# Kernel tuning notes

Hardware: AMD Instinct MI355X
Metric: run time of the kernel (lower is better)

The kernel has to match this reference:

```python
import jax, jax.numpy as jnp
import numpy as np

B, T, E, H = 2, 2048, 1024, 16
D = E // H          # head_size = 64
DF = 4 * E          # FFN inner dim


def setup_inputs() -> dict:
    key = jax.random.key(0)
    ks = jax.random.split(key, 10)
    s = E ** -0.5
    return {
        "x":  jax.random.normal(ks[0], (B, T, E), jnp.float32),
        "Wq": jax.random.normal(ks[1], (H, E, D), jnp.float32) * s,
        "Wk": jax.random.normal(ks[2], (H, E, D), jnp.float32) * s,
        "Wv": jax.random.normal(ks[3], (H, E, D), jnp.float32) * s,
        "Wo": jax.random.normal(ks[4], (E, E), jnp.float32) * s,
        "bo": jnp.zeros((E,), jnp.float32),
        "W1": jax.random.normal(ks[5], (E, DF), jnp.float32) * s,
        "b1": jnp.zeros((DF,), jnp.float32),
        "W2": jax.random.normal(ks[6], (DF, E), jnp.float32) * (DF ** -0.5),
        "b2": jnp.zeros((E,), jnp.float32),
    }


def reference(x, Wq, Wk, Wv, Wo, bo, W1, b1, W2, b2):
    Bx, Tx, C = x.shape
    # NOTE: source scales by C**-0.5 where C = n_embed (not head_size) -- faithful.
    scale = C ** -0.5
    q = jnp.einsum('btc,hcd->bhtd', x, Wq)
    k = jnp.einsum('btc,hcd->bhtd', x, Wk)
    v = jnp.einsum('btc,hcd->bhtd', x, Wv)
    scores = jnp.einsum('bhtd,bhsd->bhts', q, k) * scale   # [B,H,T,T]
    causal = jnp.tril(jnp.ones((Tx, Tx), bool))
    scores = jnp.where(causal, scores, -jnp.inf)
    attn = jax.nn.softmax(scores, axis=-1)
    out = jnp.einsum('bhts,bhsd->bhtd', attn, v)
    out = out.transpose(0, 2, 1, 3).reshape(Bx, Tx, C)     # concat heads
    x = x + (out @ Wo + bo)                                # residual + projection
    h = jax.nn.relu(x @ W1 + b1)
    x = x + (h @ W2 + b2)                                  # residual + FFN
    return x
```

## Files before the change

kernel.cpp:

```cpp
#include <hip/hip_runtime.h>

#define B_ 2
#define T_ 2048
#define E_ 1024
#define H_ 16
#define D_ 64
#define DF_ 4096
#define M_ (B_*T_)
#define NQKV_ 3072

typedef unsigned short u16;
typedef __attribute__((ext_vector_type(8))) short short8;
typedef __attribute__((ext_vector_type(4))) float f32x4;
typedef __attribute__((ext_vector_type(16))) float f32x16;

__device__ __forceinline__ u16 f2bf(float f) {
  unsigned u = __builtin_bit_cast(unsigned, f);
  u += 0x7FFFu + ((u >> 16) & 1u);
  return (u16)(u >> 16);
}
__device__ __forceinline__ unsigned pack2bf(float a, float b) {
  return (unsigned)f2bf(a) | ((unsigned)f2bf(b) << 16);
}
__device__ __forceinline__ float bf2f(u16 u) {
  return __builtin_bit_cast(float, (unsigned)u << 16);
}

__device__ __forceinline__ void gload_lds16(const u16* g, u16* l) {
  __builtin_amdgcn_global_load_lds((const __attribute__((address_space(1))) void*)g,
                                   (__attribute__((address_space(3))) void*)l, 16, 0, 0);
}

__global__ __launch_bounds__(256) void cast_bf16_kernel(const float* __restrict__ in,
                                                        u16* __restrict__ out, int n4) {
  int i = blockIdx.x * 256 + threadIdx.x;
  if (i >= n4) return;
  float4 v = ((const float4*)in)[i];
  uint2 r;
  r.x = (unsigned)f2bf(v.x) | ((unsigned)f2bf(v.y) << 16);
  r.y = (unsigned)f2bf(v.z) | ((unsigned)f2bf(v.w) << 16);
  ((uint2*)out)[i] = r;
}

__global__ __launch_bounds__(256) void transpose_cast_kernel(const float* __restrict__ in,
                                                             u16* __restrict__ out,
                                                             int R, int C, int outld) {
  __shared__ float tile[32][33];
  int z = blockIdx.z;
  int c0 = blockIdx.x * 32, r0 = blockIdx.y * 32;
  int tx = threadIdx.x & 31, ty = threadIdx.x >> 5;
  const float* ip = in + (size_t)z * R * C;
#pragma unroll
  for (int i = 0; i < 32; i += 8)
    tile[ty + i][tx] = ip[(size_t)(r0 + ty + i) * C + (c0 + tx)];
  __syncthreads();
#pragma unroll
  for (int i = 0; i < 32; i += 8)
    out[(size_t)(z * C + c0 + ty + i) * outld + (r0 + tx)] = f2bf(tile[tx][ty + i]);
}

__global__ __launch_bounds__(256) void transpose_u16_kernel(const u16* __restrict__ in,
                                                            u16* __restrict__ out,
                                                            int R, int C, int ldin) {
  __shared__ __attribute__((aligned(16))) u16 tile[64][72];
  int c0 = blockIdx.x * 64, r0 = blockIdx.y * 64;
  int t = threadIdx.x;
  int tr = t >> 4, tc = (t & 15) * 4;
#pragma unroll
  for (int i = 0; i < 4; i++)
    *(uint2*)&tile[tr + i * 16][tc] = *(const uint2*)&in[(size_t)(r0 + tr + i * 16) * ldin + c0 + tc];
  __syncthreads();
  int rr = (t & 15) * 4, cc0 = t >> 4;
#pragma unroll
  for (int i = 0; i < 4; i++) {
    int cc = cc0 + i * 16;
    u16 a = tile[rr][cc], b = tile[rr + 1][cc], c = tile[rr + 2][cc], d = tile[rr + 3][cc];
    uint2 v;
    v.x = (unsigned)a | ((unsigned)b << 16);
    v.y = (unsigned)c | ((unsigned)d << 16);
    *(uint2*)&out[(size_t)(c0 + cc) * R + r0 + rr] = v;
  }
}

template<int TM, int TN, bool BIAS, bool RELU, bool RES, bool OF32, bool OBF>
__global__ __launch_bounds__(256, 2)
void gemm_bt(const u16* __restrict__ A,
             const u16* __restrict__ Bt,
             int M, int N, int K, int lda, int ldb,
             const float* __restrict__ bias,
             const float* __restrict__ res,
             float* __restrict__ outf,
             u16* __restrict__ outb) {
  constexpr int MF = TM / 32;
  constexpr int NF = TN / 32;
  __shared__ __attribute__((aligned(16))) u16 As[2][TM][32];
  __shared__ __attribute__((aligned(16))) u16 Bs[2][TN][32];
  int m0 = blockIdx.y * TM, n0 = blockIdx.x * TN;
  int z = blockIdx.z;
  A  += (size_t)z * K;
  Bt += (size_t)z * K;
  if (OF32 && outf) outf += (size_t)z * M * N;
  if (OBF && outb)  outb += (size_t)z * M * N;
  int tid = threadIdx.x;
  int lane = tid & 63, w = tid >> 6;
  int wr = w >> 1, wc = w & 1;
  int lg = lane >> 4, lq = lane & 15;
  int srow = lane >> 2, scol = (lane & 3) * 8;

  const u16* aS0; const u16* aS1 = nullptr;
  if constexpr (TM == 128) {
    aS0 = &A[(size_t)(m0 + w * 32 +      srow) * lda + scol];
    aS1 = &A[(size_t)(m0 + w * 32 + 16 + srow) * lda + scol];
  } else {
    aS0 = &A[(size_t)(m0 + w * 16 + srow) * lda + scol];
  }
  const u16* bS0; const u16* bS1 = nullptr;
  if constexpr (TN == 128) {
    bS0 = &Bt[(size_t)(n0 + w * 32 +      srow) * ldb + scol];
    bS1 = &Bt[(size_t)(n0 + w * 32 + 16 + srow) * ldb + scol];
  } else {
    bS0 = &Bt[(size_t)(n0 + w * 16 + srow) * ldb + scol];
  }

  auto stage = [&](int buf, int k0) {
    if constexpr (TM == 128) {
      gload_lds16(aS0 + k0, &As[buf][w * 32][0]);
      gload_lds16(aS1 + k0, &As[buf][w * 32 + 16][0]);
    } else {
      gload_lds16(aS0 + k0, &As[buf][w * 16][0]);
    }
    if constexpr (TN == 128) {
      gload_lds16(bS0 + k0, &Bs[buf][w * 32][0]);
      gload_lds16(bS1 + k0, &Bs[buf][w * 32 + 16][0]);
    } else {
      gload_lds16(bS0 + k0, &Bs[buf][w * 16][0]);
    }
  };

  f32x4 acc[MF][NF] = {};

  stage(0, 0);
  __syncthreads();
  int cur = 0;
  for (int k0 = 0; k0 < K; k0 += 32) {
    if (k0 + 32 < K) stage(cur ^ 1, k0 + 32);
    short8 af[MF], bf[NF];
#pragma unroll
    for (int m = 0; m < MF; m++) af[m] = *(const short8*)&As[cur][wr * (TM / 2) + m * 16 + lq][lg * 8];
#pragma unroll
    for (int n = 0; n < NF; n++) bf[n] = *(const short8*)&Bs[cur][wc * (TN / 2) + n * 16 + lq][lg * 8];
#pragma unroll
    for (int m = 0; m < MF; m++)
#pragma unroll
      for (int n = 0; n < NF; n++)
        acc[m][n] = __builtin_amdgcn_mfma_f32_16x16x32_bf16(af[m], bf[n], acc[m][n], 0, 0, 0);
    __syncthreads();
    cur ^= 1;
  }

#pragma unroll
  for (int m = 0; m < MF; m++)
#pragma unroll
    for (int n = 0; n < NF; n++) {
      int row = m0 + wr * (TM / 2) + m * 16 + lg * 4;
      int col = n0 + wc * (TN / 2) + n * 16 + lq;
      float bv = BIAS ? bias[col] : 0.f;
#pragma unroll
      for (int r = 0; r < 4; r++) {
        float v = acc[m][n][r];
        if (BIAS) v += bv;
        if (RES)  v += res[(size_t)(row + r) * N + col];
        if (RELU) v = fmaxf(v, 0.f);
        if (OF32) outf[(size_t)(row + r) * N + col] = v;
        if (OBF)  outb[(size_t)(row + r) * N + col] = f2bf(v);
      }
    }
}

__global__ __launch_bounds__(256) void reduce2_kernel(const float* __restrict__ x1,
                                                      const u16* __restrict__ p0,
                                                      const u16* __restrict__ p1,
                                                      const float* __restrict__ b2,
                                                      float* __restrict__ out) {
  int i = blockIdx.x * 256 + threadIdx.x;
  float4 xv = ((const float4*)x1)[i];
  ushort4 a = ((const ushort4*)p0)[i];
  ushort4 b = ((const ushort4*)p1)[i];
  const float4 bb = *(const float4*)&b2[(i * 4) & (E_ - 1)];
  float4 r;
  r.x = xv.x + bf2f(a.x) + bf2f(b.x) + bb.x;
  r.y = xv.y + bf2f(a.y) + bf2f(b.y) + bb.y;
  r.z = xv.z + bf2f(a.z) + bf2f(b.z) + bb.z;
  r.w = xv.w + bf2f(a.w) + bf2f(b.w) + bb.w;
  ((float4*)out)[i] = r;
}

__global__ __launch_bounds__(256) void attn_kernel(const u16* __restrict__ qkv,
                                                   const u16* __restrict__ Vt,
                                                   u16* __restrict__ attn) {
  __shared__ __attribute__((aligned(16))) u16 Ks[64 * 64];
  __shared__ __attribute__((aligned(16))) u16 Vs[64 * 64];
  int bid = blockIdx.x;
  int pp = bid >> 8, rrb = bid & 255;
  int h  = rrb >> 4;
  int jj = rrb & 15;
  int b  = pp;
  int qt = pp ? (15 - jj) : jj;
  int tid = threadIdx.x;
  int lane = tid & 63, w = tid >> 6;
  int l31 = lane & 31, hh = lane >> 5;
  int q0w = qt * 128 + w * 32;
  int q_abs = q0w + l31;

  short8 qf[4];
  const u16* Qrow = qkv + (size_t)(b * T_ + q_abs) * NQKV_ + h * 64;
#pragma unroll
  for (int ks = 0; ks < 4; ks++) qf[ks] = *(const short8*)&Qrow[ks * 16 + hh * 8];

  const u16* Kbase  = qkv + (size_t)(b * T_) * NQKV_ + 1024 + h * 64;
  const u16* Vtbase = Vt + (size_t)(h * 64) * M_ + b * T_;

  int r0s = tid >> 3, c0s = tid & 7;
  int r1s = r0s + 32;
  unsigned kd0 = (unsigned)((r0s * 128 + c0s * 16) ^ ((r0s & 7) << 4));
  unsigned kd1 = (unsigned)((r1s * 128 + c0s * 16) ^ ((r1s & 7) << 4));
  const u16* Kg0 = &Kbase[(size_t)r0s * NQKV_ + c0s * 8];
  const u16* Kg1 = &Kbase[(size_t)r1s * NQKV_ + c0s * 8];
  const u16* Vg0 = &Vtbase[(size_t)r0s * M_ + c0s * 8];
  const u16* Vg1 = &Vtbase[(size_t)r1s * M_ + c0s * 8];

  f32x16 o[2] = {};
  float m_run = -__builtin_inff(), l_run = 0.f;
  const float SCL = 0.03125f;
  const int s_stop = qt * 128 + 128;

  uint4 kr0 = *(const uint4*)Kg0;
  uint4 kr1 = *(const uint4*)Kg1;
  uint4 vr0 = *(const uint4*)Vg0;
  uint4 vr1 = *(const uint4*)Vg1;

  for (int s0 = 0; s0 < s_stop; s0 += 64) {
    __syncthreads();
    *(uint4*)((char*)Ks + kd0) = kr0;
    *(uint4*)((char*)Ks + kd1) = kr1;
    *(uint4*)((char*)Vs + kd0) = vr0;
    *(uint4*)((char*)Vs + kd1) = vr1;
    if (s0 + 64 < s_stop) {
      kr0 = *(const uint4*)&Kg0[(size_t)(s0 + 64) * NQKV_];
      kr1 = *(const uint4*)&Kg1[(size_t)(s0 + 64) * NQKV_];
      vr0 = *(const uint4*)&Vg0[s0 + 64];
      vr1 = *(const uint4*)&Vg1[s0 + 64];
    }
    __syncthreads();
    if (s0 > q0w + 31) continue;

    f32x16 st[2];
#pragma unroll
    for (int c = 0; c < 2; c++) {
      f32x16 acc = {};
      int key = c * 32 + l31;
#pragma unroll
      for (int ks = 0; ks < 4; ks++) {
        unsigned off = (unsigned)((key * 128 + ks * 32 + hh * 16) ^ ((key & 7) << 4));
        short8 kf = *(const short8*)((const char*)Ks + off);
        acc = __builtin_amdgcn_mfma_f32_32x32x16_bf16(kf, qf[ks], acc, 0, 0, 0);
      }
      st[c] = acc;
    }

    float tmax = -__builtin_inff();
    if (s0 + 63 > q0w) {
#pragma unroll
      for (int c = 0; c < 2; c++)
#pragma unroll
        for (int r = 0; r < 16; r++) {
          int key = s0 + c * 32 + (r & 3) + 8 * (r >> 2) + 4 * hh;
          float v = (key > q_abs) ? -__builtin_inff() : st[c][r];
          st[c][r] = v;
          tmax = fmaxf(tmax, v);
        }
    } else {
#pragma unroll
      for (int c = 0; c < 2; c++)
#pragma unroll
        for (int r = 0; r < 16; r++) tmax = fmaxf(tmax, st[c][r]);
    }
    tmax = fmaxf(tmax, __shfl_xor(tmax, 32));

    if (!__all(tmax - m_run <= 256.0f)) {
      float newm = fmaxf(m_run, tmax);
      float fac = __expf((m_run - newm) * SCL);
      l_run *= fac;
      o[0] *= fac;
      o[1] *= fac;
      m_run = newm;
    }
    float nm = -m_run * SCL;
    float psum = 0.f;
#pragma unroll
    for (int c = 0; c < 2; c++)
#pragma unroll
      for (int r = 0; r < 16; r++) {
        float pv = __expf(fmaf(st[c][r], SCL, nm));
        st[c][r] = pv;
        psum += pv;
      }
    psum += __shfl_xor(psum, 32);
    l_run += psum;

    unsigned wds[2][8];
#pragma unroll
    for (int c = 0; c < 2; c++)
#pragma unroll
      for (int i = 0; i < 8; i++)
        wds[c][i] = pack2bf(st[c][2 * i], st[c][2 * i + 1]);

#pragma unroll
    for (int ks16 = 0; ks16 < 4; ks16++) {
      int c = ks16 >> 1, e = ks16 & 1;
      unsigned send0 = hh ? wds[c][4 * e]     : wds[c][4 * e + 2];
      unsigned send1 = hh ? wds[c][4 * e + 1] : wds[c][4 * e + 3];
      unsigned recv0 = (unsigned)__shfl_xor((int)send0, 32);
      unsigned recv1 = (unsigned)__shfl_xor((int)send1, 32);
      uint4 fw;
      fw.x = hh ? recv0 : wds[c][4 * e];
      fw.y = hh ? recv1 : wds[c][4 * e + 1];
      fw.z = hh ? wds[c][4 * e + 2] : recv0;
      fw.w = hh ? wds[c][4 * e + 3] : recv1;
      short8 pf = __builtin_bit_cast(short8, fw);
#pragma unroll
      for (int dc = 0; dc < 2; dc++) {
        int d = dc * 32 + l31;
        unsigned off = (unsigned)((d * 128 + ks16 * 32 + hh * 16) ^ ((d & 7) << 4));
        short8 vf = *(const short8*)((const char*)Vs + off);
        o[dc] = __builtin_amdgcn_mfma_f32_32x32x16_bf16(vf, pf, o[dc], 0, 0, 0);
      }
    }
  }

  float inv = 1.f / l_run;
  const size_t orow = (size_t)(b * T_ + q_abs) * E_ + h * 64;
#pragma unroll
  for (int dc = 0; dc < 2; dc++)
#pragma unroll
    for (int a = 0; a < 4; a++) {
      uint2 r;
      r.x = pack2bf(o[dc][4 * a] * inv, o[dc][4 * a + 1] * inv);
      r.y = pack2bf(o[dc][4 * a + 2] * inv, o[dc][4 * a + 3] * inv);
      *(uint2*)&attn[orow + dc * 32 + 8 * a + 4 * hh] = r;
    }
}

extern "C" void kernel_launch(void* const* d_in, const int* in_sizes, int n_in,
                              void* d_out, int out_size, void* d_ws, size_t ws_size,
                              hipStream_t stream) {
  const float* x  = (const float*)d_in[0];
  const float* Wq = (const float*)d_in[1];
  const float* Wk = (const float*)d_in[2];
  const float* Wv = (const float*)d_in[3];
  const float* Wo = (const float*)d_in[4];
  const float* bo = (const float*)d_in[5];
  const float* W1 = (const float*)d_in[6];
  const float* b1 = (const float*)d_in[7];
  const float* W2 = (const float*)d_in[8];
  const float* b2 = (const float*)d_in[9];
  float* out = (float*)d_out;

  const size_t MB = 1048576;
  char* ws = (char*)d_ws;
  u16* xb    = (u16*)(ws + 0);
  u16* WqkvT = (u16*)(ws + 8 * MB);
  u16* WoT   = (u16*)(ws + 14 * MB);
  u16* W1T   = (u16*)(ws + 16 * MB);
  u16* W2T   = (u16*)(ws + 24 * MB);
  u16* qkv   = (u16*)(ws + 32 * MB);
  u16* attn  = (u16*)(ws + 56 * MB);
  float* x1  = (float*)(ws + 64 * MB);
  u16* Vtb   = (u16*)(ws + 64 * MB);
  u16* x1b   = (u16*)(ws + 0);
  u16* hbuf  = (u16*)(ws + 32 * MB);
  u16* pbuf  = (u16*)(ws + 0);

  cast_bf16_kernel<<<(M_ * E_ / 4 + 255) / 256, 256, 0, stream>>>(x, xb, M_ * E_ / 4);
  transpose_cast_kernel<<<dim3(2, 32, 16),  256, 0, stream>>>(Wq, WqkvT,                E_, D_, E_);
  transpose_cast_kernel<<<dim3(2, 32, 16),  256, 0, stream>>>(Wk, WqkvT + 1024 * 1024,  E_, D_, E_);
  transpose_cast_kernel<<<dim3(2, 32, 16),  256, 0, stream>>>(Wv, WqkvT + 2048 * 1024,  E_, D_, E_);
  transpose_cast_kernel<<<dim3(32, 32, 1),  256, 0, stream>>>(Wo, WoT, E_, E_, E_);
  transpose_cast_kernel<<<dim3(128, 32, 1), 256, 0, stream>>>(W1, W1T, E_, DF_, E_);
  transpose_cast_kernel<<<dim3(32, 128, 1), 256, 0, stream>>>(W2, W2T, DF_, E_, DF_);

  gemm_bt<128,128,false,false,false,false,true><<<dim3(NQKV_ / 128, M_ / 128), 256, 0, stream>>>(
      xb, WqkvT, M_, NQKV_, E_, E_, E_, nullptr, nullptr, nullptr, qkv);

  transpose_u16_kernel<<<dim3(E_ / 64, M_ / 64), 256, 0, stream>>>(qkv + 2048, Vtb, M_, E_, NQKV_);

  attn_kernel<<<B_ * H_ * (T_ / 128), 256, 0, stream>>>(qkv, Vtb, attn);

  gemm_bt<64,128,true,false,true,true,true><<<dim3(E_ / 128, M_ / 64), 256, 0, stream>>>(
      attn, WoT, M_, E_, E_, E_, E_, bo, x, x1, x1b);
  gemm_bt<128,128,true,true,false,false,true><<<dim3(DF_ / 128, M_ / 128), 256, 0, stream>>>(
      x1b, W1T, M_, DF_, E_, E_, E_, b1, nullptr, nullptr, hbuf);
  gemm_bt<128,128,false,false,false,false,true><<<dim3(E_ / 128, M_ / 128, 2), 256, 0, stream>>>(
      hbuf, W2T, M_, E_, DF_ / 2, DF_, DF_, nullptr, nullptr, nullptr, pbuf);
  reduce2_kernel<<<M_ * E_ / 4 / 256, 256, 0, stream>>>(x1, pbuf, pbuf + (size_t)M_ * E_, b2, out);
}
```

Baseline: 248.8 us.

## Deepen GEMM K-tile with XOR-swizzled LDS, hardware bf16 pack, and attention MFMA priority

The GEMM K-step grows from 32 to 64 per stage, and the LDS tiles use an XOR column swizzle on both the global-to-LDS load and the fragment reads to cut bank conflicts. Barrier count per K drops while LDS use doubles. Software bf16 rounding is replaced with the v_cvt_pk_bf16_f32 instruction in the GEMM epilogue and the attention kernel. The attention kernel also raises wave priority around its MFMA blocks and uses tree reductions for the row max and row sum, which shortens dependency chains. Doubling LDS may reduce occupancy.

```diff
diff --git a/kernel.cpp b/kernel.cpp
--- a/kernel.cpp
+++ b/kernel.cpp
@@ -22,8 +22,29 @@
 __device__ __forceinline__ unsigned pack2bf(float a, float b) {
   return (unsigned)f2bf(a) | ((unsigned)f2bf(b) << 16);
 }
+__device__ __forceinline__ unsigned cvtpk(float a, float b) {
+  unsigned r;
+  asm("v_cvt_pk_bf16_f32 %0, %1, %2" : "=v"(r) : "v"(a), "v"(b));
+  return r;
+}
 __device__ __forceinline__ float bf2f(u16 u) {
   return __builtin_bit_cast(float, (unsigned)u << 16);
+}
+__device__ __forceinline__ float vmax16(const f32x16& v) {
+  float a0 = fmaxf(v[0], v[1]),   a1 = fmaxf(v[2], v[3]);
+  float a2 = fmaxf(v[4], v[5]),   a3 = fmaxf(v[6], v[7]);
+  float a4 = fmaxf(v[8], v[9]),   a5 = fmaxf(v[10], v[11]);
+  float a6 = fmaxf(v[12], v[13]), a7 = fmaxf(v[14], v[15]);
+  float b0 = fmaxf(a0, a1), b1 = fmaxf(a2, a3), b2 = fmaxf(a4, a5), b3 = fmaxf(a6, a7);
+  return fmaxf(fmaxf(b0, b1), fmaxf(b2, b3));
+}
+__device__ __forceinline__ float vsum16(const f32x16& v) {
+  float a0 = v[0] + v[1],   a1 = v[2] + v[3];
+  float a2 = v[4] + v[5],   a3 = v[6] + v[7];
+  float a4 = v[8] + v[9],   a5 = v[10] + v[11];
+  float a6 = v[12] + v[13], a7 = v[14] + v[15];
+  float b0 = a0 + a1, b1 = a2 + a3, b2 = a4 + a5, b3 = a6 + a7;
+  return (b0 + b1) + (b2 + b3);
 }
 
 __device__ __forceinline__ void gload_lds16(const u16* g, u16* l) {
@@ -93,8 +114,10 @@
              u16* __restrict__ outb) {
   constexpr int MF = TM / 32;
   constexpr int NF = TN / 32;
-  __shared__ __attribute__((aligned(16))) u16 As[2][TM][32];
-  __shared__ __attribute__((aligned(16))) u16 Bs[2][TN][32];
+  constexpr int ACH = TM / 32;
+  constexpr int BCH = TN / 32;
+  __shared__ __attribute__((aligned(16))) u16 As[2][TM][64];
+  __shared__ __attribute__((aligned(16))) u16 Bs[2][TN][64];
   int m0 = blockIdx.y * TM, n0 = blockIdx.x * TN;
   int z = blockIdx.z;
   A  += (size_t)z * K;
@@ -105,55 +128,49 @@
   int lane = tid & 63, w = tid >> 6;
   int wr = w >> 1, wc = w & 1;
   int lg = lane >> 4, lq = lane & 15;
-  int srow = lane >> 2, scol = (lane & 3) * 8;
-
-  const u16* aS0; const u16* aS1 = nullptr;
-  if constexpr (TM == 128) {
-    aS0 = &A[(size_t)(m0 + w * 32 +      srow) * lda + scol];
-    aS1 = &A[(size_t)(m0 + w * 32 + 16 + srow) * lda + scol];
-  } else {
-    aS0 = &A[(size_t)(m0 + w * 16 + srow) * lda + scol];
-  }
-  const u16* bS0; const u16* bS1 = nullptr;
-  if constexpr (TN == 128) {
-    bS0 = &Bt[(size_t)(n0 + w * 32 +      srow) * ldb + scol];
-    bS1 = &Bt[(size_t)(n0 + w * 32 + 16 + srow) * ldb + scol];
-  } else {
-    bS0 = &Bt[(size_t)(n0 + w * 16 + srow) * ldb + scol];
-  }
+  int srow8 = lane >> 3;
+  int scolsw = ((lane & 7) ^ srow8) * 8;
+
+  const u16* aSrcP[ACH];
+  const u16* bSrcP[BCH];
+#pragma unroll
+  for (int j = 0; j < ACH; j++)
+    aSrcP[j] = &A[(size_t)(m0 + w * (ACH * 8) + j * 8 + srow8) * lda + scolsw];
+#pragma unroll
+  for (int j = 0; j < BCH; j++)
+    bSrcP[j] = &Bt[(size_t)(n0 + w * (BCH * 8) + j * 8 + srow8) * ldb + scolsw];
 
   auto stage = [&](int buf, int k0) {
-    if constexpr (TM == 128) {
-      gload_lds16(aS0 + k0, &As[buf][w * 32][0]);
-      gload_lds16(aS1 + k0, &As[buf][w * 32 + 16][0]);
-    } else {
-      gload_lds16(aS0 + k0, &As[buf][w * 16][0]);
-    }
-    if constexpr (TN == 128) {
-      gload_lds16(bS0 + k0, &Bs[buf][w * 32][0]);
-      gload_lds16(bS1 + k0, &Bs[buf][w * 32 + 16][0]);
-    } else {
-      gload_lds16(bS0 + k0, &Bs[buf][w * 16][0]);
-    }
+#pragma unroll
+    for (int j = 0; j < ACH; j++)
+      gload_lds16(aSrcP[j] + k0, &As[buf][w * (ACH * 8) + j * 8][0]);
+#pragma unroll
+    for (int j = 0; j < BCH; j++)
+      gload_lds16(bSrcP[j] + k0, &Bs[buf][w * (BCH * 8) + j * 8][0]);
   };
 
   f32x4 acc[MF][NF] = {};
+  int lqx = lq & 7;
 
   stage(0, 0);
   __syncthreads();
   int cur = 0;
-  for (int k0 = 0; k0 < K; k0 += 32) {
-    if (k0 + 32 < K) stage(cur ^ 1, k0 + 32);
-    short8 af[MF], bf[NF];
-#pragma unroll
-    for (int m = 0; m < MF; m++) af[m] = *(const short8*)&As[cur][wr * (TM / 2) + m * 16 + lq][lg * 8];
-#pragma unroll
-    for (int n = 0; n < NF; n++) bf[n] = *(const short8*)&Bs[cur][wc * (TN / 2) + n * 16 + lq][lg * 8];
-#pragma unroll
-    for (int m = 0; m < MF; m++)
-#pragma unroll
-      for (int n = 0; n < NF; n++)
-        acc[m][n] = __builtin_amdgcn_mfma_f32_16x16x32_bf16(af[m], bf[n], acc[m][n], 0, 0, 0);
+  for (int k0 = 0; k0 < K; k0 += 64) {
+    if (k0 + 64 < K) stage(cur ^ 1, k0 + 64);
+#pragma unroll
+    for (int kk = 0; kk < 2; kk++) {
+      short8 af[MF], bf[NF];
+      int csw = ((lg + kk * 4) ^ lqx) * 8;
+#pragma unroll
+      for (int m = 0; m < MF; m++) af[m] = *(const short8*)&As[cur][wr * (TM / 2) + m * 16 + lq][csw];
+#pragma unroll
+      for (int n = 0; n < NF; n++) bf[n] = *(const short8*)&Bs[cur][wc * (TN / 2) + n * 16 + lq][csw];
+#pragma unroll
+      for (int m = 0; m < MF; m++)
+#pragma unroll
+        for (int n = 0; n < NF; n++)
+          acc[m][n] = __builtin_amdgcn_mfma_f32_16x16x32_bf16(af[m], bf[n], acc[m][n], 0, 0, 0);
+    }
     __syncthreads();
     cur ^= 1;
   }
@@ -165,6 +182,7 @@
       int row = m0 + wr * (TM / 2) + m * 16 + lg * 4;
       int col = n0 + wc * (TN / 2) + n * 16 + lq;
       float bv = BIAS ? bias[col] : 0.f;
+      float vv[4];
 #pragma unroll
       for (int r = 0; r < 4; r++) {
         float v = acc[m][n][r];
@@ -172,7 +190,15 @@
         if (RES)  v += res[(size_t)(row + r) * N + col];
         if (RELU) v = fmaxf(v, 0.f);
         if (OF32) outf[(size_t)(row + r) * N + col] = v;
-        if (OBF)  outb[(size_t)(row + r) * N + col] = f2bf(v);
+        vv[r] = v;
+      }
+      if (OBF) {
+        unsigned p01 = cvtpk(vv[0], vv[1]);
+        unsigned p23 = cvtpk(vv[2], vv[3]);
+        outb[(size_t)(row + 0) * N + col] = (u16)p01;
+        outb[(size_t)(row + 1) * N + col] = (u16)(p01 >> 16);
+        outb[(size_t)(row + 2) * N + col] = (u16)p23;
+        outb[(size_t)(row + 3) * N + col] = (u16)(p23 >> 16);
       }
     }
 }
@@ -255,6 +281,7 @@
     if (s0 > q0w + 31) continue;
 
     f32x16 st[2];
+    __builtin_amdgcn_s_setprio(1);
 #pragma unroll
     for (int c = 0; c < 2; c++) {
       f32x16 acc = {};
@@ -267,24 +294,18 @@
       }
       st[c] = acc;
     }
-
-    float tmax = -__builtin_inff();
+    __builtin_amdgcn_s_setprio(0);
+
     if (s0 + 63 > q0w) {
 #pragma unroll
       for (int c = 0; c < 2; c++)
 #pragma unroll
         for (int r = 0; r < 16; r++) {
           int key = s0 + c * 32 + (r & 3) + 8 * (r >> 2) + 4 * hh;
-          float v = (key > q_abs) ? -__builtin_inff() : st[c][r];
-          st[c][r] = v;
-          tmax = fmaxf(tmax, v);
+          st[c][r] = (key > q_abs) ? -__builtin_inff() : st[c][r];
         }
-    } else {
-#pragma unroll
-      for (int c = 0; c < 2; c++)
-#pragma unroll
-        for (int r = 0; r < 16; r++) tmax = fmaxf(tmax, st[c][r]);
-    }
+    }
+    float tmax = fmaxf(vmax16(st[0]), vmax16(st[1]));
     tmax = fmaxf(tmax, __shfl_xor(tmax, 32));
 
     if (!__all(tmax - m_run <= 256.0f)) {
@@ -296,15 +317,12 @@
       m_run = newm;
     }
     float nm = -m_run * SCL;
-    float psum = 0.f;
 #pragma unroll
     for (int c = 0; c < 2; c++)
 #pragma unroll
-      for (int r = 0; r < 16; r++) {
-        float pv = __expf(fmaf(st[c][r], SCL, nm));
-        st[c][r] = pv;
-        psum += pv;
-      }
+      for (int r = 0; r < 16; r++)
+        st[c][r] = __expf(fmaf(st[c][r], SCL, nm));
+    float psum = vsum16(st[0]) + vsum16(st[1]);
     psum += __shfl_xor(psum, 32);
     l_run += psum;
 
@@ -313,8 +331,9 @@
     for (int c = 0; c < 2; c++)
 #pragma unroll
       for (int i = 0; i < 8; i++)
-        wds[c][i] = pack2bf(st[c][2 * i], st[c][2 * i + 1]);
-
+        wds[c][i] = cvtpk(st[c][2 * i], st[c][2 * i + 1]);
+
+    __builtin_amdgcn_s_setprio(1);
 #pragma unroll
     for (int ks16 = 0; ks16 < 4; ks16++) {
       int c = ks16 >> 1, e = ks16 & 1;
@@ -336,6 +355,7 @@
         o[dc] = __builtin_amdgcn_mfma_f32_32x32x16_bf16(vf, pf, o[dc], 0, 0, 0);
       }
     }
+    __builtin_amdgcn_s_setprio(0);
   }
 
   float inv = 1.f / l_run;
@@ -344,9 +364,11 @@
   for (int dc = 0; dc < 2; dc++)
 #pragma unroll
     for (int a = 0; a < 4; a++) {
+      float e0 = o[dc][4 * a] * inv,     e1 = o[dc][4 * a + 1] * inv;
+      float e2 = o[dc][4 * a + 2] * inv, e3 = o[dc][4 * a + 3] * inv;
       uint2 r;
-      r.x = pack2bf(o[dc][4 * a] * inv, o[dc][4 * a + 1] * inv);
-      r.y = pack2bf(o[dc][4 * a + 2] * inv, o[dc][4 * a + 3] * inv);
+      r.x = cvtpk(e0, e1);
+      r.y = cvtpk(e2, e3);
       *(uint2*)&attn[orow + dc * 32 + 8 * a + 4 * hh] = r;
     }
 }
```

After: 236.7 us. 4.9% less time.
